# Performance work log

Measured on AMD Instinct MI355X. Metric: run time of the kernel, lower is better.

## Reference

```python
import jax, jax.numpy as jnp
import numpy as np

# Longformer-base-4096 dims; attention_window=128 -> one-sided window 64
B, S, D, H, L, F, V, NUM_LABELS = 1, 4096, 768, 12, 12, 3072, 50265, 100
DH = D // H
W = 64            # one-sided sliding window
NC = S // W       # number of query chunks
EPS = 1e-5
SCALE = float(1.0 / np.sqrt(DH))


def layer_norm(x, s, b):
    m = jnp.mean(x, axis=-1, keepdims=True)
    v = jnp.mean(jnp.square(x - m), axis=-1, keepdims=True)
    return (x - m) * jax.lax.rsqrt(v + EPS) * s + b


def heads(x):  # [B,S,D] -> [B,H,S,DH]
    return x.reshape(B, S, H, DH).transpose(0, 2, 1, 3)


def chunk3(t):  # [B,H,S,DH] -> [B,H,NC,3W,DH]: key blocks c-1,c,c+1 per query chunk c
    tp = jnp.pad(t, ((0, 0), (0, 0), (W, W), (0, 0)))
    tb = tp.reshape(B, H, NC + 2, W, DH)
    return jnp.concatenate([tb[:, :, i:i + NC] for i in range(3)], axis=3)


def _forward(input_ids, attention_mask, emb_tok, emb_pos, ln_emb_scale, ln_emb_bias,
             Wq, bq, Wk, bk, Wv, bv, Wqg, bqg, Wkg, bkg, Wvg, bvg, Wo, bo,
             ln1_scale, ln1_bias, Wf1, bf1, Wf2, bf2, ln2_scale, ln2_bias, Wc, bc):
    am = attention_mask > 0                      # [B,S]
    x = layer_norm(emb_tok[input_ids] + emb_pos[None, :, :], ln_emb_scale, ln_emb_bias)

    # static sliding-window masks, shared by all layers
    qi = jnp.arange(W)[:, None]
    kj = jnp.arange(3 * W)[None, :]
    band = (kj >= qi) & (kj <= qi + 2 * W)       # |key - query| <= W within a chunk triple
    kvalid = am & (jnp.arange(S)[None, :] > 0)   # global token (pos 0) excluded from window
    kp = jnp.pad(kvalid, ((0, 0), (W, W))).reshape(B, NC + 2, W)
    kmask = jnp.concatenate([kp[:, i:i + NC] for i in range(3)], axis=2)   # [B,NC,3W]
    win_mask = band[None, None, None] & kmask[:, None, :, None, :]         # [B,1,NC,W,3W]

    def layer(x, p):
        (wq, bq_, wk, bk_, wv, bv_, wqg, bqg_, wkg, bkg_, wvg, bvg_, wo, bo_,
         l1s, l1b, wf1, bf1_, wf2, bf2_, l2s, l2b) = p
        q = heads(x @ wq + bq_) * SCALE
        k = heads(x @ wk + bk_)
        v = heads(x @ wv + bv_)
        qc = q.reshape(B, H, NC, W, DH)
        k3, v3 = chunk3(k), chunk3(v)
        sc = jnp.einsum('bhcqd,bhckd->bhcqk', qc, k3)          # [B,H,NC,W,3W]
        sc = jnp.where(win_mask, sc, -1e9)
        # every token also attends to the global CLS key (standard K/V of pos 0)
        sg = jnp.einsum('bhsd,bhd->bhs', q, k[:, :, 0]).reshape(B, H, NC, W, 1)
        probs = jax.nn.softmax(jnp.concatenate([sg, sc], axis=-1), axis=-1)
        pg, pl = probs[..., 0], probs[..., 1:]
        ctx = jnp.einsum('bhcqk,bhckd->bhcqd', pl, v3).reshape(B, H, S, DH)
        ctx = ctx + pg.reshape(B, H, S, 1) * v[:, :, :1]
        # global token attends to everything with its own (global) projections
        qg = heads(x @ wqg + bqg_)[:, :, 0] * SCALE            # [B,H,DH]
        kg = heads(x @ wkg + bkg_)
        vg = heads(x @ wvg + bvg_)
        sgl = jnp.where(am[:, None, :], jnp.einsum('bhd,bhjd->bhj', qg, kg), -1e9)
        ctx0 = jnp.einsum('bhj,bhjd->bhd', jax.nn.softmax(sgl, axis=-1), vg)
        ctx = ctx.at[:, :, 0].set(ctx0)
        attn = ctx.transpose(0, 2, 1, 3).reshape(B, S, D) @ wo + bo_
        x1 = layer_norm(x + attn, l1s, l1b)
        h = jax.nn.gelu(x1 @ wf1 + bf1_, approximate=False)
        return layer_norm(x1 + h @ wf2 + bf2_, l2s, l2b), None

    params = (Wq, bq, Wk, bk, Wv, bv, Wqg, bqg, Wkg, bkg, Wvg, bvg, Wo, bo,
              ln1_scale, ln1_bias, Wf1, bf1, Wf2, bf2, ln2_scale, ln2_bias)
    x, _ = jax.lax.scan(layer, x, params)
    return x[:, 0] @ Wc + bc                                   # [B, NUM_LABELS]


def setup_inputs():
    key = jax.random.key(0)
    ks = jax.random.split(key, 40)
    it = iter(range(40))
    nrm = lambda shape: jax.random.normal(ks[next(it)], shape, dtype=jnp.float32) * 0.02
    z = lambda shape: jnp.zeros(shape, jnp.float32)
    o = lambda shape: jnp.ones(shape, jnp.float32)
    return {
        'input_ids': jax.random.randint(ks[next(it)], (B, S), 0, V, dtype=jnp.int32),
        'attention_mask': jnp.ones((B, S), dtype=jnp.int32),
        'emb_tok': nrm((V, D)), 'emb_pos': nrm((S, D)),
        'ln_emb_scale': o((D,)), 'ln_emb_bias': z((D,)),
        'Wq': nrm((L, D, D)), 'bq': z((L, D)),
        'Wk': nrm((L, D, D)), 'bk': z((L, D)),
        'Wv': nrm((L, D, D)), 'bv': z((L, D)),
        'Wqg': nrm((L, D, D)), 'bqg': z((L, D)),
        'Wkg': nrm((L, D, D)), 'bkg': z((L, D)),
        'Wvg': nrm((L, D, D)), 'bvg': z((L, D)),
        'Wo': nrm((L, D, D)), 'bo': z((L, D)),
        'ln1_scale': o((L, D)), 'ln1_bias': z((L, D)),
        'Wf1': nrm((L, D, F)), 'bf1': z((L, F)),
        'Wf2': nrm((L, F, D)), 'bf2': z((L, D)),
        'ln2_scale': o((L, D)), 'ln2_bias': z((L, D)),
        'Wc': nrm((D, NUM_LABELS)), 'bc': z((NUM_LABELS,)),
    }


def reference(input_ids, attention_mask, emb_tok, emb_pos, ln_emb_scale, ln_emb_bias,
              Wq, bq, Wk, bk, Wv, bv, Wqg, bqg, Wkg, bkg, Wvg, bvg, Wo, bo,
              ln1_scale, ln1_bias, Wf1, bf1, Wf2, bf2, ln2_scale, ln2_bias, Wc, bc):
    return _forward(input_ids, attention_mask, emb_tok, emb_pos, ln_emb_scale, ln_emb_bias,
                    Wq, bq, Wk, bk, Wv, bv, Wqg, bqg, Wkg, bkg, Wvg, bvg, Wo, bo,
                    ln1_scale, ln1_bias, Wf1, bf1, Wf2, bf2, ln2_scale, ln2_bias, Wc, bc)
```

## Files before the change

kernel.cpp:

```cpp
#include <hip/hip_runtime.h>
#include <hip/hip_bf16.h>

typedef unsigned short u16;
typedef __attribute__((ext_vector_type(8))) short bf16x8;
typedef __attribute__((ext_vector_type(4))) float f32x4;

constexpr int S = 4096, D = 768, H = 12, NL = 12, F = 3072, NLAB = 100, DH = 64;
constexpr int NQKV = 3840;
constexpr float SCALE = 0.125f;
constexpr float EPS = 1e-5f;

__device__ __forceinline__ float bits2f(u16 u) {
  union { unsigned int i; float f; } x; x.i = ((unsigned int)u) << 16; return x.f;
}
__device__ __forceinline__ u16 f2bbits(float f) {
  union { float f; unsigned int i; } x; x.f = f;
  return (u16)((x.i + 0x7FFFu + ((x.i >> 16) & 1u)) >> 16);
}
__device__ __forceinline__ float rdw(const void* p, size_t i, int isf32) {
  return isf32 ? ((const float*)p)[i] : bits2f(((const u16*)p)[i]);
}
__device__ __forceinline__ void gload16(const void* g, void* l) {
  __builtin_amdgcn_global_load_lds(
      (const __attribute__((address_space(1))) void*)g,
      (__attribute__((address_space(3))) void*)l, 16, 0, 0);
}

__global__ void detect_k(const void* lns, int* flag) {
  *flag = (*(const unsigned int*)lns == 0x3F800000u) ? 1 : 0;
}

struct PrepArgs {
  const void *Wq, *Wk, *Wv, *Wkg, *Wvg, *Wo, *Wqg, *Wf1, *Wf2;
  const void *bq, *bk, *bv, *bkg, *bvg, *bo, *bqg, *bf1, *bf2;
  u16 *wt_qkv, *wt_o, *wt_qg, *wt_f1, *wt_f2;
  float* biasb;
  const int* flag;
};
constexpr int PPL = 8676;

__global__ __launch_bounds__(256) void prep_all(PrepArgs a)
{
  const int l = blockIdx.x / PPL;
  const int b = blockIdx.x % PPL;
  const int t = threadIdx.x;
  const int isf32 = *a.flag;
  const size_t oDD = (size_t)l * D * D, oDF = (size_t)l * D * F;
  const size_t oD = (size_t)l * D, oF = (size_t)l * F;
  float* bb = a.biasb + (size_t)l * 9216;

  if (b < 8640) {
    __shared__ float tile[32][33];
    const void* src; size_t soff; int N, ld, rowoff, n0, k0;
    u16* dst; float scl = 1.f;
    if (b < 4032) {
      const int m = b / 576, ti = b - m * 576;
      soff = oDD; N = D; ld = D; rowoff = 0;
      switch (m) {
        case 0:  src = a.Wq;  dst = a.wt_qkv + (size_t)l * NQKV * D; scl = SCALE;  break;
        case 1:  src = a.Wk;  dst = a.wt_qkv + (size_t)l * NQKV * D; rowoff = 768; break;
        case 2:  src = a.Wv;  dst = a.wt_qkv + (size_t)l * NQKV * D; rowoff = 1536; break;
        case 3:  src = a.Wkg; dst = a.wt_qkv + (size_t)l * NQKV * D; rowoff = 2304; break;
        case 4:  src = a.Wvg; dst = a.wt_qkv + (size_t)l * NQKV * D; rowoff = 3072; break;
        case 5:  src = a.Wo;  dst = a.wt_o   + (size_t)l * D * D;    break;
        default: src = a.Wqg; dst = a.wt_qg  + (size_t)l * D * D;    scl = SCALE;  break;
      }
      n0 = (ti % 24) * 32; k0 = (ti / 24) * 32;
    } else if (b < 6336) {
      const int ti = b - 4032;
      src = a.Wf1; soff = oDF; N = F; dst = a.wt_f1 + (size_t)l * F * D; rowoff = 0; ld = D;
      n0 = (ti % 96) * 32; k0 = (ti / 96) * 32;
    } else {
      const int ti = b - 6336;
      src = a.Wf2; soff = oDF; N = D; dst = a.wt_f2 + (size_t)l * D * F; rowoff = 0; ld = F;
      n0 = (ti % 24) * 32; k0 = (ti / 24) * 32;
    }
    const int r = t >> 3, cc = (t & 7) << 2;
    const size_t si = soff + (size_t)(k0 + r) * N + n0 + cc;
    if (isf32) {
      const float4 v = *reinterpret_cast<const float4*>(&((const float*)src)[si]);
      tile[r][cc] = v.x * scl; tile[r][cc+1] = v.y * scl;
      tile[r][cc+2] = v.z * scl; tile[r][cc+3] = v.w * scl;
    } else {
      const ushort4 v = *reinterpret_cast<const ushort4*>(&((const u16*)src)[si]);
      tile[r][cc] = bits2f(v.x) * scl; tile[r][cc+1] = bits2f(v.y) * scl;
      tile[r][cc+2] = bits2f(v.z) * scl; tile[r][cc+3] = bits2f(v.w) * scl;
    }
    __syncthreads();
    const ushort4 ov = make_ushort4(f2bbits(tile[cc+0][r]), f2bbits(tile[cc+1][r]),
                                    f2bbits(tile[cc+2][r]), f2bbits(tile[cc+3][r]));
    *reinterpret_cast<ushort4*>(&dst[(size_t)(rowoff + n0 + r) * ld + k0 + cc]) = ov;
  } else {
    const int i = (b - 8640) * 256 + t;
    float v;
    if      (i < 768)  v = rdw(a.bq,  oD + i,        isf32) * SCALE;
    else if (i < 1536) v = rdw(a.bk,  oD + i - 768,  isf32);
    else if (i < 2304) v = rdw(a.bv,  oD + i - 1536, isf32);
    else if (i < 3072) v = rdw(a.bkg, oD + i - 2304, isf32);
    else if (i < 3840) v = rdw(a.bvg, oD + i - 3072, isf32);
    else if (i < 4608) v = rdw(a.bo,  oD + i - 3840, isf32);
    else if (i < 7680) v = rdw(a.bf1, oF + i - 4608, isf32);
    else if (i < 8448) v = rdw(a.bf2, oD + i - 7680, isf32);
    else               v = rdw(a.bqg, oD + i - 8448, isf32) * SCALE;
    bb[i] = v;
  }
}

__global__ __launch_bounds__(512) void gemm256(
    const u16* __restrict__ A, const u16* __restrict__ BT,
    const float* __restrict__ bias, u16* __restrict__ Cb,
    int M, int N, int K, int act)
{
  __shared__ u16 smem[49152];
  const int t = threadIdx.x;
  const int wid = t >> 6, lane = t & 63;
  const int wm = wid >> 2, wn = wid & 3;
  const int m0 = blockIdx.y * 256, n0 = blockIdx.x * 256;
  const int nt = K >> 5;

  const int srow = lane >> 2;
  const int skc = (lane & 3) << 3;

  auto stage = [&](int kt, int b) {
#pragma unroll
    for (int j = 0; j < 4; ++j) {
      const int half = j & 1;
      const int row = half * 128 + wid * 16 + srow;
      const u16* src = (j < 2)
          ? &A [(size_t)(m0 + row) * K + kt * 32 + skc]
          : &BT[(size_t)(n0 + row) * K + kt * 32 + skc];
      gload16(src, &smem[b * 16384 + (j >= 2 ? 8192 : 0) + half * 4096 + wid * 512]);
    }
  };

  f32x4 acc[8][4];
#pragma unroll
  for (int mf = 0; mf < 8; ++mf)
#pragma unroll
    for (int nf = 0; nf < 4; ++nf)
      acc[mf][nf] = (f32x4){0.f, 0.f, 0.f, 0.f};

  const int frow = lane & 15;
  const int fkb = (lane >> 4) << 3;

  stage(0, 0);
  stage(1, 1);
  asm volatile("s_waitcnt vmcnt(4)" ::: "memory");
  __builtin_amdgcn_s_barrier();

  for (int kt = 0; kt < nt; ++kt) {
    const int rb = (kt % 3) * 16384;
    bf16x8 Af[8], Bf[4];
#pragma unroll
    for (int mf = 0; mf < 8; ++mf)
      Af[mf] = *reinterpret_cast<const bf16x8*>(
          &smem[rb + (wm * 128 + mf * 16 + frow) * 32 + fkb]);
#pragma unroll
    for (int nf = 0; nf < 4; ++nf)
      Bf[nf] = *reinterpret_cast<const bf16x8*>(
          &smem[rb + 8192 + (wn * 64 + nf * 16 + frow) * 32 + fkb]);

    if (kt + 2 < nt) stage(kt + 2, (kt + 2) % 3);

    asm volatile("s_waitcnt lgkmcnt(0)" ::: "memory");
    __builtin_amdgcn_sched_barrier(0);
    __builtin_amdgcn_s_setprio(1);
#pragma unroll
    for (int mf = 0; mf < 8; ++mf)
#pragma unroll
      for (int nf = 0; nf < 4; ++nf)
        acc[mf][nf] = __builtin_amdgcn_mfma_f32_16x16x32_bf16(Af[mf], Bf[nf], acc[mf][nf], 0, 0, 0);
    __builtin_amdgcn_s_setprio(0);

    if (kt < nt - 2)       asm volatile("s_waitcnt vmcnt(4)" ::: "memory");
    else if (kt == nt - 2) asm volatile("s_waitcnt vmcnt(0)" ::: "memory");
    __builtin_amdgcn_s_barrier();
  }

  const int crow = (lane >> 4) << 2;
  const int ccol = lane & 15;
#pragma unroll
  for (int mf = 0; mf < 8; ++mf) {
#pragma unroll
    for (int nf = 0; nf < 4; ++nf) {
      const int gc = n0 + wn * 64 + nf * 16 + ccol;
      const float bv = bias[gc];
#pragma unroll
      for (int r = 0; r < 4; ++r) {
        const int gr = m0 + wm * 128 + mf * 16 + crow + r;
        float x = acc[mf][nf][r] + bv;
        if (act) x = 0.5f * x * (1.0f + erff(x * 0.70710678118654752f));
        Cb[(size_t)gr * N + gc] = f2bbits(x);
      }
    }
  }
}

template<int BN, int SPLITK>
__global__ __launch_bounds__(256) void mfma_gemm(
    const u16* __restrict__ A, const u16* __restrict__ BT,
    const float* __restrict__ bias,
    float* __restrict__ Cf, u16* __restrict__ Cb,
    int M, int N, int K, int act)
{
  constexpr int BM = 128, BK = 32;
  constexpr int WN = BN / 2;
  constexpr int NR = WN / 16;
  __shared__ u16 As[BM * BK];
  __shared__ u16 Bs[BN * BK];
  const int t = threadIdx.x;
  const int wid = t >> 6, lane = t & 63;
  const int wr = wid >> 1, wc = wid & 1;
  const int m0 = blockIdx.y * BM, n0 = blockIdx.x * BN;
  const int z = (SPLITK > 1) ? blockIdx.z : 0;
  const int kLen = K / SPLITK;
  const int k0 = z * kLen;
  const int l_row = lane >> 2;
  const int l_kc = (lane & 3) << 3;

  f32x4 acc[4][NR];
#pragma unroll
  for (int m = 0; m < 4; ++m)
#pragma unroll
    for (int n = 0; n < NR; ++n)
      acc[m][n] = (f32x4){0.f, 0.f, 0.f, 0.f};

  const int frow = lane & 15;
  const int fkb = (lane >> 4) << 3;

  for (int kt = k0; kt < k0 + kLen; kt += BK) {
#pragma unroll
    for (int i = 0; i < 2; ++i) {
      const int ch = wid * 2 + i;
      gload16(&A[(size_t)(m0 + ch * 16 + l_row) * K + kt + l_kc], &As[ch * 512]);
    }
#pragma unroll
    for (int i = 0; i < BN / 64; ++i) {
      const int ch = wid * (BN / 64) + i;
      gload16(&BT[(size_t)(n0 + ch * 16 + l_row) * K + kt + l_kc], &Bs[ch * 512]);
    }
    __syncthreads();
    bf16x8 af[4], bfr[NR];
#pragma unroll
    for (int m = 0; m < 4; ++m)
      af[m] = *reinterpret_cast<const bf16x8*>(&As[(wr * 64 + m * 16 + frow) * BK + fkb]);
#pragma unroll
    for (int n = 0; n < NR; ++n)
      bfr[n] = *reinterpret_cast<const bf16x8*>(&Bs[(wc * WN + n * 16 + frow) * BK + fkb]);
#pragma unroll
    for (int m = 0; m < 4; ++m)
#pragma unroll
      for (int n = 0; n < NR; ++n)
        acc[m][n] = __builtin_amdgcn_mfma_f32_16x16x32_bf16(af[m], bfr[n], acc[m][n], 0, 0, 0);
    __syncthreads();
  }

  float* Cp = (SPLITK > 1) ? (Cf + (size_t)z * M * N) : Cf;
  const int crow = (lane >> 4) << 2;
  const int ccol = lane & 15;
#pragma unroll
  for (int m = 0; m < 4; ++m) {
#pragma unroll
    for (int n = 0; n < NR; ++n) {
      const int gc = n0 + wc * WN + n * 16 + ccol;
      const float bv = (z == 0) ? bias[gc] : 0.f;
#pragma unroll
      for (int r = 0; r < 4; ++r) {
        const int gr = m0 + wr * 64 + m * 16 + crow + r;
        float x = acc[m][n][r] + bv;
        if (SPLITK == 1 && act) x = 0.5f * x * (1.0f + erff(x * 0.70710678118654752f));
        if (Cp) Cp[(size_t)gr * N + gc] = x;
        if (SPLITK == 1 && Cb) Cb[(size_t)gr * N + gc] = f2bbits(x);
      }
    }
  }
}

__global__ void embed_k(const int* __restrict__ ids, const void* __restrict__ tok,
                        const void* __restrict__ pos, float* __restrict__ out,
                        const int* __restrict__ flag)
{
  const int isf32 = *flag;
  const int s = blockIdx.x, t = threadIdx.x;
  const int id = ids[s];
  for (int c = t; c < D; c += 256)
    out[(size_t)s * D + c] = rdw(tok, (size_t)id * D + c, isf32) + rdw(pos, (size_t)s * D + c, isf32);
}

__global__ __launch_bounds__(256) void ln_res_k(
    const float* __restrict__ Ain,
    const float* __restrict__ P0, const float* __restrict__ P1,
    const void* __restrict__ g, size_t goff, const void* __restrict__ b, size_t boff,
    float* __restrict__ Out, u16* __restrict__ Outb, const int* __restrict__ flag)
{
  const int isf32 = *flag;
  const int w = threadIdx.x >> 6, lane = threadIdx.x & 63;
  const int r = blockIdx.x * 4 + w;
  const size_t rb = (size_t)r * D;
  float v[12];
  float ls = 0.f;
#pragma unroll
  for (int j = 0; j < 3; ++j) {
    const int c = lane * 4 + j * 256;
    float4 x = *reinterpret_cast<const float4*>(&Ain[rb + c]);
    if (P0) { const float4 p = *reinterpret_cast<const float4*>(&P0[rb + c]);
              x.x += p.x; x.y += p.y; x.z += p.z; x.w += p.w; }
    if (P1) { const float4 p = *reinterpret_cast<const float4*>(&P1[rb + c]);
              x.x += p.x; x.y += p.y; x.z += p.z; x.w += p.w; }
    v[j*4+0] = x.x; v[j*4+1] = x.y; v[j*4+2] = x.z; v[j*4+3] = x.w;
    ls += x.x + x.y + x.z + x.w;
  }
#pragma unroll
  for (int off = 32; off; off >>= 1) ls += __shfl_xor(ls, off);
  const float mean = ls * (1.0f / D);
  float lv = 0.f;
#pragma unroll
  for (int e = 0; e < 12; ++e) { const float dd = v[e] - mean; lv += dd * dd; }
#pragma unroll
  for (int off = 32; off; off >>= 1) lv += __shfl_xor(lv, off);
  const float rstd = rsqrtf(lv * (1.0f / D) + EPS);
#pragma unroll
  for (int j = 0; j < 3; ++j) {
    const int c = lane * 4 + j * 256;
    float o[4];
#pragma unroll
    for (int e = 0; e < 4; ++e)
      o[e] = (v[j*4+e] - mean) * rstd * rdw(g, goff + c + e, isf32) + rdw(b, boff + c + e, isf32);
    *reinterpret_cast<float4*>(&Out[rb + c]) = make_float4(o[0], o[1], o[2], o[3]);
    if (Outb)
      *reinterpret_cast<ushort4*>(&Outb[rb + c]) =
          make_ushort4(f2bbits(o[0]), f2bbits(o[1]), f2bbits(o[2]), f2bbits(o[3]));
  }
}

__global__ __launch_bounds__(256) void qg_gemv(
    const u16* __restrict__ Xb, const u16* __restrict__ WgT,
    const float* __restrict__ biasb, float* __restrict__ QG)
{
  const int wid = threadIdx.x >> 6, lane = threadIdx.x & 63;
  const int o = blockIdx.x * 4 + wid;
  float a = 0.f;
#pragma unroll
  for (int j = 0; j < 12; ++j) {
    const int k = j * 64 + lane;
    a += bits2f(Xb[k]) * bits2f(WgT[(size_t)o * 768 + k]);
  }
#pragma unroll
  for (int off = 32; off; off >>= 1) a += __shfl_xor(a, off);
  if (lane == 0) QG[o] = a + biasb[8448 + o];
}

__global__ __launch_bounds__(256) void win_attn3(
    const u16* __restrict__ QKV, const int* __restrict__ am, u16* __restrict__ CTXb)
{
  __shared__ u16 Ql[64 * 64];
  __shared__ u16 Kl[224 * 64];
  __shared__ u16 Vt[64 * 232];
  __shared__ int kwin[224];
  const int c = blockIdx.x, h = blockIdx.y;
  const int t = threadIdx.x, w = t >> 6, lane = t & 63;
  const int base = c * 64 - 64, s0 = c * 64;

  for (int i = t; i < 1024; i += 256) {
    const int r = i >> 4, c4 = (i & 15) << 2;
    const ushort4 v = *reinterpret_cast<const ushort4*>(
        &QKV[(size_t)(s0 + r) * NQKV + h * 64 + c4]);
    *reinterpret_cast<ushort4*>((char*)Ql + ((r * 128 + c4 * 2) ^ ((r & 7) << 4))) = v;
  }
  for (int i = t; i < 3584; i += 256) {
    const int r = i >> 4, c4 = (i & 15) << 2;
    const int kp = (r < 192) ? (base + r) : ((r == 192) ? 0 : -1);
    ushort4 v = make_ushort4(0, 0, 0, 0);
    if (kp >= 0 && kp < S)
      v = *reinterpret_cast<const ushort4*>(&QKV[(size_t)kp * NQKV + 768 + h * 64 + c4]);
    *reinterpret_cast<ushort4*>((char*)Kl + ((r * 128 + c4 * 2) ^ ((r & 7) << 4))) = v;
  }
  for (int i = t; i < 3584; i += 256) {
    const int r = i >> 4, c4 = (i & 15) << 2;
    const int kp = (r < 192) ? (base + r) : ((r == 192) ? 0 : -1);
    ushort4 v = make_ushort4(0, 0, 0, 0);
    if (kp >= 0 && kp < S)
      v = *reinterpret_cast<const ushort4*>(&QKV[(size_t)kp * NQKV + 1536 + h * 64 + c4]);
    Vt[(c4 + 0) * 232 + r] = v.x;
    Vt[(c4 + 1) * 232 + r] = v.y;
    Vt[(c4 + 2) * 232 + r] = v.z;
    Vt[(c4 + 3) * 232 + r] = v.w;
  }
  if (t < 224) {
    const int kp = base + t;
    kwin[t] = (t < 192 && kp >= 1 && kp < S) ? am[kp] : 0;
  }
  __syncthreads();

  const int frow = lane & 15, fkb = (lane >> 4) << 3;
  const int crow = (lane >> 4) << 2, ccol = lane & 15;
  const int qrow = w * 16 + frow;

  bf16x8 aq[2];
#pragma unroll
  for (int ks = 0; ks < 2; ++ks)
    aq[ks] = *reinterpret_cast<const bf16x8*>(
        (const char*)Ql + ((qrow * 128 + (ks * 32 + fkb) * 2) ^ ((qrow & 7) << 4)));

  f32x4 sc[14];
#pragma unroll
  for (int tl = 0; tl < 14; ++tl) {
    sc[tl] = (f32x4){0.f, 0.f, 0.f, 0.f};
    const int key = tl * 16 + frow;
#pragma unroll
    for (int ks = 0; ks < 2; ++ks) {
      const bf16x8 bk = *reinterpret_cast<const bf16x8*>(
          (const char*)Kl + ((key * 128 + (ks * 32 + fkb) * 2) ^ ((key & 7) << 4)));
      sc[tl] = __builtin_amdgcn_mfma_f32_16x16x32_bf16(aq[ks], bk, sc[tl], 0, 0, 0);
    }
  }

  float m4[4] = {-1e30f, -1e30f, -1e30f, -1e30f};
#pragma unroll
  for (int tl = 0; tl < 14; ++tl) {
    const int kidx = tl * 16 + ccol;
    const int kw = kwin[kidx];
    const bool isg = (kidx == 192);
#pragma unroll
    for (int r = 0; r < 4; ++r) {
      const int qi = w * 16 + crow + r;
      const bool valid = isg || ((kidx >= qi) && (kidx <= qi + 128) && kw);
      const float v = valid ? sc[tl][r] : -1e30f;
      sc[tl][r] = v;
      m4[r] = fmaxf(m4[r], v);
    }
  }
#pragma unroll
  for (int r = 0; r < 4; ++r)
#pragma unroll
    for (int off = 8; off; off >>= 1) m4[r] = fmaxf(m4[r], __shfl_xor(m4[r], off));

  float ssum[4] = {0.f, 0.f, 0.f, 0.f};
#pragma unroll
  for (int tl = 0; tl < 14; ++tl)
#pragma unroll
    for (int r = 0; r < 4; ++r) {
      const float e = __expf(sc[tl][r] - m4[r]);
      sc[tl][r] = e;
      ssum[r] += e;
    }
#pragma unroll
  for (int r = 0; r < 4; ++r)
#pragma unroll
    for (int off = 8; off; off >>= 1) ssum[r] += __shfl_xor(ssum[r], off);

  __syncthreads();
  u16* Pl = Kl;
#pragma unroll
  for (int tl = 0; tl < 14; ++tl) {
    const int kidx = tl * 16 + ccol;
#pragma unroll
    for (int r = 0; r < 4; ++r) {
      const int row = crow + r;
      *(u16*)((char*)Pl + w * 7168 + ((row * 448 + kidx * 2) ^ ((row & 7) << 4))) =
          f2bbits(sc[tl][r]);
    }
  }
  __syncthreads();

  bf16x8 pa[7];
#pragma unroll
  for (int ks = 0; ks < 7; ++ks)
    pa[ks] = *reinterpret_cast<const bf16x8*>(
        (const char*)Pl + w * 7168 + ((frow * 448 + (ks * 32 + fkb) * 2) ^ ((frow & 7) << 4)));

  f32x4 av[4];
#pragma unroll
  for (int n = 0; n < 4; ++n) {
    av[n] = (f32x4){0.f, 0.f, 0.f, 0.f};
#pragma unroll
    for (int ks = 0; ks < 7; ++ks) {
      const bf16x8 bv = *reinterpret_cast<const bf16x8*>(&Vt[(n * 16 + frow) * 232 + ks * 32 + fkb]);
      av[n] = __builtin_amdgcn_mfma_f32_16x16x32_bf16(pa[ks], bv, av[n], 0, 0, 0);
    }
  }
  float inv[4];
#pragma unroll
  for (int r = 0; r < 4; ++r) inv[r] = 1.f / ssum[r];
#pragma unroll
  for (int n = 0; n < 4; ++n)
#pragma unroll
    for (int r = 0; r < 4; ++r) {
      const int s = s0 + w * 16 + crow + r;
      CTXb[(size_t)s * D + h * 64 + n * 16 + ccol] = f2bbits(av[n][r] * inv[r]);
    }
}

__global__ __launch_bounds__(256) void glob_part(
    const u16* __restrict__ QKV, const float* __restrict__ QG,
    const int* __restrict__ am, float* __restrict__ gp)
{
  __shared__ float qsh[DH];
  __shared__ float se[256];
  __shared__ float red[4];
  __shared__ float part[4][DH];
  const int seg = blockIdx.x, h = blockIdx.y, t = threadIdx.x;
  const int j0 = seg * 256;
  if (t < DH) qsh[t] = QG[h * DH + t];
  __syncthreads();
  const int j = j0 + t;
  float a = 0.f;
  const u16* kr = &QKV[(size_t)j * NQKV + 2304 + h * 64];
#pragma unroll
  for (int v8 = 0; v8 < 8; ++v8) {
    const bf16x8 kv = *reinterpret_cast<const bf16x8*>(&kr[v8 * 8]);
#pragma unroll
    for (int e = 0; e < 8; ++e)
      a += qsh[v8 * 8 + e] * bits2f((u16)kv[e]);
  }
  a = (am[j] > 0) ? a : -1e9f;
  float m = a;
#pragma unroll
  for (int off = 32; off; off >>= 1) m = fmaxf(m, __shfl_xor(m, off));
  if ((t & 63) == 0) red[t >> 6] = m;
  __syncthreads();
  m = fmaxf(fmaxf(red[0], red[1]), fmaxf(red[2], red[3]));
  const float e = __expf(a - m);
  se[t] = e;
  float ls = e;
#pragma unroll
  for (int off = 32; off; off >>= 1) ls += __shfl_xor(ls, off);
  __syncthreads();
  if ((t & 63) == 0) red[t >> 6] = ls;
  __syncthreads();
  const float lsum = red[0] + red[1] + red[2] + red[3];
  const int g = t >> 6, d = t & 63;
  float acc = 0.f;
  for (int jj = g; jj < 256; jj += 4)
    acc += se[jj] * bits2f(QKV[(size_t)(j0 + jj) * NQKV + 3072 + h * 64 + d]);
  part[g][d] = acc;
  __syncthreads();
  if (t < 64) {
    float* o = &gp[(size_t)(h * 16 + seg) * 66];
    o[t] = part[0][t] + part[1][t] + part[2][t] + part[3][t];
    if (t == 0) { o[64] = m; o[65] = lsum; }
  }
}

__global__ void glob_comb(const float* __restrict__ gp, u16* __restrict__ CTXb)
{
  const int h = blockIdx.x, t = threadIdx.x;
  float M = -1e30f;
  for (int i = 0; i < 16; ++i) M = fmaxf(M, gp[(size_t)(h * 16 + i) * 66 + 64]);
  float L = 0.f, acc = 0.f;
  for (int i = 0; i < 16; ++i) {
    const float* o = &gp[(size_t)(h * 16 + i) * 66];
    const float w = __expf(o[64] - M);
    L += o[65] * w;
    acc += o[t] * w;
  }
  CTXb[h * 64 + t] = f2bbits(acc / L);
}

__global__ __launch_bounds__(256) void cls_k(
    const float* __restrict__ X, const void* __restrict__ Wc,
    const void* __restrict__ bc, void* __restrict__ out,
    const int* __restrict__ flag)
{
  const int isf32 = *flag;
  const int wid = threadIdx.x >> 6, lane = threadIdx.x & 63;
  const int n = blockIdx.x * 4 + wid;
  if (n >= NLAB) return;
  float a = 0.f;
#pragma unroll
  for (int j = 0; j < 12; ++j) {
    const int k = j * 64 + lane;
    a += X[k] * rdw(Wc, (size_t)k * NLAB + n, isf32);
  }
#pragma unroll
  for (int off = 32; off; off >>= 1) a += __shfl_xor(a, off);
  if (lane == 0) {
    a += rdw(bc, n, isf32);
    if (isf32) ((float*)out)[n] = a;
    else ((u16*)out)[n] = f2bbits(a);
  }
}

extern "C" void kernel_launch(void* const* d_in, const int* in_sizes, int n_in,
                              void* d_out, int out_size, void* d_ws, size_t ws_size,
                              hipStream_t stream)
{
  const int*  ids = (const int*)d_in[0];
  const int*  am  = (const int*)d_in[1];
  const void* emb_tok = d_in[2];
  const void* emb_pos = d_in[3];
  const void* ln_e_g  = d_in[4];
  const void* ln_e_b  = d_in[5];
  const void* Wq  = d_in[6];  const void* bq  = d_in[7];
  const void* Wk  = d_in[8];  const void* bk  = d_in[9];
  const void* Wv  = d_in[10]; const void* bv  = d_in[11];
  const void* Wqg = d_in[12]; const void* bqg = d_in[13];
  const void* Wkg = d_in[14]; const void* bkg = d_in[15];
  const void* Wvg = d_in[16]; const void* bvg = d_in[17];
  const void* Wo  = d_in[18]; const void* bo  = d_in[19];
  const void* l1g = d_in[20]; const void* l1b = d_in[21];
  const void* Wf1 = d_in[22]; const void* bf1 = d_in[23];
  const void* Wf2 = d_in[24]; const void* bf2 = d_in[25];
  const void* l2g = d_in[26]; const void* l2b = d_in[27];
  const void* Wc  = d_in[28]; const void* bc  = d_in[29];

  float* ws = (float*)d_ws;
  const size_t SD = (size_t)S * D;
  size_t cur = 0;
  auto af32 = [&](size_t n) { float* p = ws + cur; cur += n; return p; };
  auto au16 = [&](size_t n_u16) { u16* p = (u16*)(ws + cur); cur += (n_u16 + 1) / 2; return p; };

  float* X     = af32(SD);
  float* X1    = af32(SD);
  float* TMP   = af32(2 * SD);
  u16*   QKV16 = au16(5 * SD);
  u16*   Hb    = au16((size_t)S * F);
  u16*   Xb    = au16(SD);
  u16*   X1b   = au16(SD);
  u16*   CTXb  = au16(SD);
  u16*   wt_qkv = au16((size_t)NL * NQKV * D);
  u16*   wt_o   = au16((size_t)NL * D * D);
  u16*   wt_qg  = au16((size_t)NL * D * D);
  u16*   wt_f1  = au16((size_t)NL * F * D);
  u16*   wt_f2  = au16((size_t)NL * D * F);
  float* biasb  = af32((size_t)NL * 9216);
  float* QGb    = af32(768);
  float* gp     = af32((size_t)H * 16 * 66);
  int*   flag   = (int*)af32(4);

  float* T0 = TMP;
  float* T1 = TMP + SD;

  detect_k<<<1, 1, 0, stream>>>(ln_e_g, flag);

  PrepArgs pa;
  pa.Wq = Wq; pa.Wk = Wk; pa.Wv = Wv; pa.Wkg = Wkg; pa.Wvg = Wvg;
  pa.Wo = Wo; pa.Wqg = Wqg; pa.Wf1 = Wf1; pa.Wf2 = Wf2;
  pa.bq = bq; pa.bk = bk; pa.bv = bv; pa.bkg = bkg; pa.bvg = bvg;
  pa.bo = bo; pa.bqg = bqg; pa.bf1 = bf1; pa.bf2 = bf2;
  pa.wt_qkv = wt_qkv; pa.wt_o = wt_o; pa.wt_qg = wt_qg;
  pa.wt_f1 = wt_f1; pa.wt_f2 = wt_f2; pa.biasb = biasb; pa.flag = flag;
  prep_all<<<NL * PPL, 256, 0, stream>>>(pa);

  embed_k<<<S, 256, 0, stream>>>(ids, emb_tok, emb_pos, T0, flag);
  ln_res_k<<<S / 4, 256, 0, stream>>>(T0, nullptr, nullptr,
                                      ln_e_g, 0, ln_e_b, 0, X, Xb, flag);

  for (int l = 0; l < NL; ++l) {
    const size_t oD = (size_t)l * D;
    u16* wqkv_l = wt_qkv + (size_t)l * NQKV * D;
    u16* wo_l   = wt_o   + (size_t)l * D * D;
    u16* wqg_l  = wt_qg  + (size_t)l * D * D;
    u16* wf1_l  = wt_f1  + (size_t)l * F * D;
    u16* wf2_l  = wt_f2  + (size_t)l * D * F;
    float* bb_l = biasb + (size_t)l * 9216;

    gemm256<<<dim3(NQKV / 256, S / 256), 512, 0, stream>>>(
        Xb, wqkv_l, bb_l, QKV16, S, NQKV, D, 0);
    qg_gemv<<<192, 256, 0, stream>>>(Xb, wqg_l, bb_l, QGb);
    win_attn3<<<dim3(S / 64, H), 256, 0, stream>>>(QKV16, am, CTXb);
    glob_part<<<dim3(16, H), 256, 0, stream>>>(QKV16, QGb, am, gp);
    glob_comb<<<H, 64, 0, stream>>>(gp, CTXb);
    mfma_gemm<64, 2><<<dim3(D / 64, S / 128, 2), 256, 0, stream>>>(
        CTXb, wo_l, bb_l + 3840, TMP, nullptr, S, D, D, 0);
    ln_res_k<<<S / 4, 256, 0, stream>>>(X, T0, T1,
                                        l1g, oD, l1b, oD, X1, X1b, flag);
    gemm256<<<dim3(F / 256, S / 256), 512, 0, stream>>>(
        X1b, wf1_l, bb_l + 4608, Hb, S, F, D, 1);
    mfma_gemm<64, 2><<<dim3(D / 64, S / 128, 2), 256, 0, stream>>>(
        Hb, wf2_l, bb_l + 7680, TMP, nullptr, S, D, F, 0);
    ln_res_k<<<S / 4, 256, 0, stream>>>(X1, T0, T1,
                                        l2g, oD, l2b, oD, X, Xb, flag);
  }
  cls_k<<<25, 256, 0, stream>>>(X, Wc, bc, d_out, flag);
}
```

Baseline: 3.097 ms.

## Fuse global-query GEMV and combine into global attention; split-K gemm256 for FFN2

Removes the separate qg_gemv and glob_comb kernels. Each global-attention block now recomputes its head's 64-wide global query projection, and the last block per head, found through an atomic counter, does the softmax combine. The FFN down-projection moves from the 128-tile mfma_gemm to the 256x256 gemm256 with a split-K=2 template path that writes fp32 partials. The goal is fewer launches and a more efficient GEMM tile, at the cost of redundant GEMV work (16x per head) and a grid of only 96 blocks for FFN2.

```diff
diff --git a/kernel.cpp b/kernel.cpp
--- a/kernel.cpp
+++ b/kernel.cpp
@@ -26,8 +26,10 @@
       (__attribute__((address_space(3))) void*)l, 16, 0, 0);
 }
 
-__global__ void detect_k(const void* lns, int* flag) {
-  *flag = (*(const unsigned int*)lns == 0x3F800000u) ? 1 : 0;
+__global__ void detect_k(const void* lns, int* flag, int* cnt) {
+  const int t = threadIdx.x;
+  if (t == 0) *flag = (*(const unsigned int*)lns == 0x3F800000u) ? 1 : 0;
+  if (t < 16) cnt[t] = 0;
 }
 
 struct PrepArgs {
@@ -106,9 +108,10 @@
   }
 }
 
+template<int SPLITK>
 __global__ __launch_bounds__(512) void gemm256(
     const u16* __restrict__ A, const u16* __restrict__ BT,
-    const float* __restrict__ bias, u16* __restrict__ Cb,
+    const float* __restrict__ bias, float* __restrict__ Cf, u16* __restrict__ Cb,
     int M, int N, int K, int act)
 {
   __shared__ u16 smem[49152];
@@ -116,7 +119,10 @@
   const int wid = t >> 6, lane = t & 63;
   const int wm = wid >> 2, wn = wid & 3;
   const int m0 = blockIdx.y * 256, n0 = blockIdx.x * 256;
-  const int nt = K >> 5;
+  const int z = (SPLITK > 1) ? blockIdx.z : 0;
+  const int kLen = K / SPLITK;
+  const int kof = z * kLen;
+  const int nt = kLen >> 5;
 
   const int srow = lane >> 2;
   const int skc = (lane & 3) << 3;
@@ -127,8 +133,8 @@
       const int half = j & 1;
       const int row = half * 128 + wid * 16 + srow;
       const u16* src = (j < 2)
-          ? &A [(size_t)(m0 + row) * K + kt * 32 + skc]
-          : &BT[(size_t)(n0 + row) * K + kt * 32 + skc];
+          ? &A [(size_t)(m0 + row) * K + kof + kt * 32 + skc]
+          : &BT[(size_t)(n0 + row) * K + kof + kt * 32 + skc];
       gload16(src, &smem[b * 16384 + (j >= 2 ? 8192 : 0) + half * 4096 + wid * 512]);
     }
   };
@@ -184,13 +190,17 @@
 #pragma unroll
     for (int nf = 0; nf < 4; ++nf) {
       const int gc = n0 + wn * 64 + nf * 16 + ccol;
-      const float bv = bias[gc];
+      const float bv = (z == 0) ? bias[gc] : 0.f;
 #pragma unroll
       for (int r = 0; r < 4; ++r) {
         const int gr = m0 + wm * 128 + mf * 16 + crow + r;
         float x = acc[mf][nf][r] + bv;
-        if (act) x = 0.5f * x * (1.0f + erff(x * 0.70710678118654752f));
-        Cb[(size_t)gr * N + gc] = f2bbits(x);
+        if (SPLITK == 1) {
+          if (act) x = 0.5f * x * (1.0f + erff(x * 0.70710678118654752f));
+          Cb[(size_t)gr * N + gc] = f2bbits(x);
+        } else {
+          (Cf + (size_t)z * M * N)[(size_t)gr * N + gc] = x;
+        }
       }
     }
   }
@@ -333,23 +343,6 @@
   }
 }
 
-__global__ __launch_bounds__(256) void qg_gemv(
-    const u16* __restrict__ Xb, const u16* __restrict__ WgT,
-    const float* __restrict__ biasb, float* __restrict__ QG)
-{
-  const int wid = threadIdx.x >> 6, lane = threadIdx.x & 63;
-  const int o = blockIdx.x * 4 + wid;
-  float a = 0.f;
-#pragma unroll
-  for (int j = 0; j < 12; ++j) {
-    const int k = j * 64 + lane;
-    a += bits2f(Xb[k]) * bits2f(WgT[(size_t)o * 768 + k]);
-  }
-#pragma unroll
-  for (int off = 32; off; off >>= 1) a += __shfl_xor(a, off);
-  if (lane == 0) QG[o] = a + biasb[8448 + o];
-}
-
 __global__ __launch_bounds__(256) void win_attn3(
     const u16* __restrict__ QKV, const int* __restrict__ am, u16* __restrict__ CTXb)
 {
@@ -491,18 +484,35 @@
     }
 }
 
-__global__ __launch_bounds__(256) void glob_part(
-    const u16* __restrict__ QKV, const float* __restrict__ QG,
-    const int* __restrict__ am, float* __restrict__ gp)
+__global__ __launch_bounds__(256) void glob_attn2(
+    const u16* __restrict__ Xb, const u16* __restrict__ WgT,
+    const float* __restrict__ bb, const u16* __restrict__ QKV,
+    const int* __restrict__ am, float* __restrict__ gp,
+    int* __restrict__ cnt, u16* __restrict__ CTXb)
 {
   __shared__ float qsh[DH];
   __shared__ float se[256];
   __shared__ float red[4];
   __shared__ float part[4][DH];
+  __shared__ int lastflag;
   const int seg = blockIdx.x, h = blockIdx.y, t = threadIdx.x;
+  const int w = t >> 6, lane = t & 63;
   const int j0 = seg * 256;
-  if (t < DH) qsh[t] = QG[h * DH + t];
-  __syncthreads();
+
+  for (int j = 0; j < 16; ++j) {
+    const int oo = w * 16 + j, o = h * 64 + oo;
+    float a = 0.f;
+#pragma unroll
+    for (int jj = 0; jj < 12; ++jj) {
+      const int k = jj * 64 + lane;
+      a += bits2f(Xb[k]) * bits2f(WgT[(size_t)o * 768 + k]);
+    }
+#pragma unroll
+    for (int off = 32; off; off >>= 1) a += __shfl_xor(a, off);
+    if (lane == 0) qsh[oo] = a + bb[8448 + o];
+  }
+  __syncthreads();
+
   const int j = j0 + t;
   float a = 0.f;
   const u16* kr = &QKV[(size_t)j * NQKV + 2304 + h * 64];
@@ -540,21 +550,27 @@
     o[t] = part[0][t] + part[1][t] + part[2][t] + part[3][t];
     if (t == 0) { o[64] = m; o[65] = lsum; }
   }
-}
-
-__global__ void glob_comb(const float* __restrict__ gp, u16* __restrict__ CTXb)
-{
-  const int h = blockIdx.x, t = threadIdx.x;
-  float M = -1e30f;
-  for (int i = 0; i < 16; ++i) M = fmaxf(M, gp[(size_t)(h * 16 + i) * 66 + 64]);
-  float L = 0.f, acc = 0.f;
-  for (int i = 0; i < 16; ++i) {
-    const float* o = &gp[(size_t)(h * 16 + i) * 66];
-    const float w = __expf(o[64] - M);
-    L += o[65] * w;
-    acc += o[t] * w;
-  }
-  CTXb[h * 64 + t] = f2bbits(acc / L);
+  __syncthreads();
+  __threadfence();
+  if (t == 0) lastflag = (atomicAdd(&cnt[h], 1) == 15) ? 1 : 0;
+  __syncthreads();
+  if (lastflag) {
+    __threadfence();
+    if (t < 64) {
+      float M = -1e30f;
+      for (int i = 0; i < 16; ++i) M = fmaxf(M, gp[(size_t)(h * 16 + i) * 66 + 64]);
+      float L = 0.f, a2 = 0.f;
+      for (int i = 0; i < 16; ++i) {
+        const float* o = &gp[(size_t)(h * 16 + i) * 66];
+        const float wgt = __expf(o[64] - M);
+        L += o[65] * wgt;
+        a2 += o[t] * wgt;
+      }
+      CTXb[h * 64 + t] = f2bbits(a2 / L);
+    }
+    __syncthreads();
+    if (t == 0) atomicExch(&cnt[h], 0);
+  }
 }
 
 __global__ __launch_bounds__(256) void cls_k(
@@ -624,14 +640,14 @@
   u16*   wt_f1  = au16((size_t)NL * F * D);
   u16*   wt_f2  = au16((size_t)NL * D * F);
   float* biasb  = af32((size_t)NL * 9216);
-  float* QGb    = af32(768);
   float* gp     = af32((size_t)H * 16 * 66);
   int*   flag   = (int*)af32(4);
+  int*   cnt    = (int*)af32(16);
 
   float* T0 = TMP;
   float* T1 = TMP + SD;
 
-  detect_k<<<1, 1, 0, stream>>>(ln_e_g, flag);
+  detect_k<<<1, 32, 0, stream>>>(ln_e_g, flag, cnt);
 
   PrepArgs pa;
   pa.Wq = Wq; pa.Wk = Wk; pa.Wv = Wv; pa.Wkg = Wkg; pa.Wvg = Wvg;
@@ -655,19 +671,18 @@
     u16* wf2_l  = wt_f2  + (size_t)l * D * F;
     float* bb_l = biasb + (size_t)l * 9216;
 
-    gemm256<<<dim3(NQKV / 256, S / 256), 512, 0, stream>>>(
-        Xb, wqkv_l, bb_l, QKV16, S, NQKV, D, 0);
-    qg_gemv<<<192, 256, 0, stream>>>(Xb, wqg_l, bb_l, QGb);
+    gemm256<1><<<dim3(NQKV / 256, S / 256), 512, 0, stream>>>(
+        Xb, wqkv_l, bb_l, nullptr, QKV16, S, NQKV, D, 0);
     win_attn3<<<dim3(S / 64, H), 256, 0, stream>>>(QKV16, am, CTXb);
-    glob_part<<<dim3(16, H), 256, 0, stream>>>(QKV16, QGb, am, gp);
-    glob_comb<<<H, 64, 0, stream>>>(gp, CTXb);
+    glob_attn2<<<dim3(16, H), 256, 0, stream>>>(
+        Xb, wqg_l, bb_l, QKV16, am, gp, cnt, CTXb);
     mfma_gemm<64, 2><<<dim3(D / 64, S / 128, 2), 256, 0, stream>>>(
         CTXb, wo_l, bb_l + 3840, TMP, nullptr, S, D, D, 0);
     ln_res_k<<<S / 4, 256, 0, stream>>>(X, T0, T1,
                                         l1g, oD, l1b, oD, X1, X1b, flag);
-    gemm256<<<dim3(F / 256, S / 256), 512, 0, stream>>>(
-        X1b, wf1_l, bb_l + 4608, Hb, S, F, D, 1);
-    mfma_gemm<64, 2><<<dim3(D / 64, S / 128, 2), 256, 0, stream>>>(
+    gemm256<1><<<dim3(F / 256, S / 256), 512, 0, stream>>>(
+        X1b, wf1_l, bb_l + 4608, nullptr, Hb, S, F, D, 1);
+    gemm256<2><<<dim3(D / 256, S / 256, 2), 512, 0, stream>>>(
         Hb, wf2_l, bb_l + 7680, TMP, nullptr, S, D, F, 0);
     ln_res_k<<<S / 4, 256, 0, stream>>>(X1, T0, T1,
                                         l2g, oD, l2b, oD, X, Xb, flag);
```

Measured after the change: 3.550 ms. +14.6%, slower.
